# Kernel optimization log

Hardware: AMD Instinct MI355X
Metric: run time of the kernel (lower is better)

## Reference

```python
import jax, jax.numpy as jnp
import numpy as np

B, S, N, D, C, H = 256, 256, 128, 256, 512, 4  # batch, seq, mem_slots, mem_dim, controller_dim, heads
HD = D // H


def setup_inputs() -> dict:
    key = jax.random.key(0)
    ks = jax.random.split(key, 12)
    sc = 0.02
    p = lambda k, shape: (jax.random.normal(k, shape, jnp.float32) * sc)
    return {
        "input_seq": jax.random.normal(ks[0], (B, S, D), jnp.float32),
        "memory_init": jax.random.normal(ks[1], (N, D), jnp.float32) * (np.sqrt(6.0 / (N + D)) / np.sqrt(3.0)),
        # LSTM (torch gate order i, f, g, o)
        "W_ih": p(ks[2], (4 * C, D)), "W_hh": p(ks[3], (4 * C, C)),
        "b_ih": jnp.zeros((4 * C,), jnp.float32), "b_hh": jnp.zeros((4 * C,), jnp.float32),
        # heads
        "W_read": p(ks[4], (D, C)), "b_read": jnp.zeros((D,), jnp.float32),
        "W_write": p(ks[5], (2 * D, C)), "b_write": jnp.zeros((2 * D,), jnp.float32),
        "W_erase": p(ks[6], (D, C)), "b_erase": jnp.zeros((D,), jnp.float32),
        # MultiheadAttention packed in-proj (q,k,v) + out-proj
        "W_in": p(ks[7], (3 * D, D)), "b_in": jnp.zeros((3 * D,), jnp.float32),
        "W_out": p(ks[8], (D, D)), "b_out": jnp.zeros((D,), jnp.float32),
        # gates
        "W_rg": p(ks[9], (1, C)), "b_rg": jnp.zeros((1,), jnp.float32),
        "W_wg": p(ks[10], (1, C)), "b_wg": jnp.zeros((1,), jnp.float32),
    }


def reference(input_seq, memory_init, W_ih, W_hh, b_ih, b_hh,
              W_read, b_read, W_write, b_write, W_erase, b_erase,
              W_in, b_in, W_out, b_out, W_rg, b_rg, W_wg, b_wg):
    b, s, d = input_seq.shape
    Wq, Wk, Wv = jnp.split(W_in, 3, axis=0)
    bq, bk, bv = jnp.split(b_in, 3)
    inv_sqrt_hd = 1.0 / np.sqrt(HD)

    mem0 = jnp.broadcast_to(memory_init, (b,) + memory_init.shape)
    h0 = jnp.zeros((b, C), input_seq.dtype)
    c0 = jnp.zeros((b, C), input_seq.dtype)

    def step(carry, x_t):
        h, c, mem = carry  # h,c: [B,C]; mem: [B,N,D]
        # LSTM cell (torch gate order i,f,g,o)
        gates = x_t @ W_ih.T + b_ih + h @ W_hh.T + b_hh
        i, f, g, o = jnp.split(gates, 4, axis=-1)
        c = jax.nn.sigmoid(f) * c + jax.nn.sigmoid(i) * jnp.tanh(g)
        h = jax.nn.sigmoid(o) * jnp.tanh(c)
        # --- read: MHA(query=read_key, key=value=memory) ---
        rk = h @ W_read.T + b_read                      # [B,D]
        q = (rk @ Wq.T + bq).reshape(b, H, HD)          # [B,H,hd]
        k = (mem @ Wk.T + bk).reshape(b, -1, H, HD)     # [B,N,H,hd]
        v = (mem @ Wv.T + bv).reshape(b, -1, H, HD)
        scores = jnp.einsum('bhd,bnhd->bhn', q, k) * inv_sqrt_hd
        attn = jax.nn.softmax(scores, axis=-1)          # [B,H,N]
        ctx = jnp.einsum('bhn,bnhd->bhd', attn, v).reshape(b, d)
        read_out = ctx @ W_out.T + b_out
        read_gate = jax.nn.sigmoid(h @ W_rg.T + b_rg)   # [B,1]
        read = read_gate * read_out
        # --- write: erase/add ---
        wp = h @ W_write.T + b_write
        write_key, write_val = wp[:, :d], wp[:, d:]
        erase_vec = jax.nn.sigmoid(h @ W_erase.T + b_erase)  # [B,D]
        write_gate = jax.nn.sigmoid(h @ W_wg.T + b_wg)       # [B,1]
        wa = jax.nn.softmax(jnp.einsum('bd,bnd->bn', write_key, mem), axis=-1)  # [B,N]
        ew = wa[:, :, None]                                   # [B,N,1]
        mem = mem * (1.0 - ew * erase_vec[:, None, :]) + write_gate[:, None, :] * (ew * write_val[:, None, :])
        return (h, c, mem), x_t + read

    (hT, cT, memT), outs = jax.lax.scan(step, (h0, c0, mem0), jnp.swapaxes(input_seq, 0, 1))
    output_sequence = jnp.swapaxes(outs, 0, 1)  # [B,S,D]
    return output_sequence, memT
```

## Files before the change

### kernel.cpp

```cpp
#include <hip/hip_runtime.h>

#define S_LEN 256
#define B_SZ  256
#define N_MEM 128
#define D_DIM 256
#define C_DIM 512
#define NBLK  256
#define PROJS 1792
#define AGENT __HIP_MEMORY_SCOPE_AGENT

typedef __bf16 bf16x8 __attribute__((ext_vector_type(8)));
typedef unsigned short ushort4v __attribute__((ext_vector_type(4)));
typedef float floatx4 __attribute__((ext_vector_type(4)));
typedef float floatx2 __attribute__((ext_vector_type(2)));

__device__ __forceinline__ unsigned short f2bf(float f){
  unsigned u = __float_as_uint(f);
  u += 0x7FFFu + ((u >> 16) & 1u);
  return (unsigned short)(u >> 16);
}
__device__ __forceinline__ float bf2f(unsigned short v){
  return __uint_as_float(((unsigned)v) << 16);
}
__device__ __forceinline__ float sigm(float x){ return 1.f/(1.f + __expf(-x)); }
__device__ __forceinline__ floatx4 mfma16(bf16x8 a, bf16x8 b, floatx4 c){
  return __builtin_amdgcn_mfma_f32_16x16x32_bf16(a, b, c, 0, 0, 0);
}

__device__ __forceinline__ int msw(int n, int d){
  return (n << 8) + ((((d >> 2) ^ (n & 7)) << 2) | (d & 3));
}

__device__ __forceinline__ unsigned ald32(const void* p){
  return __hip_atomic_load((const unsigned*)p, __ATOMIC_RELAXED, AGENT);
}
__device__ __forceinline__ unsigned long long ald64(const void* p){
  return __hip_atomic_load((const unsigned long long*)p, __ATOMIC_RELAXED, AGENT);
}
__device__ __forceinline__ void ast32(void* p, unsigned v){
  __hip_atomic_store((unsigned*)p, v, __ATOMIC_RELAXED, AGENT);
}
__device__ __forceinline__ void ast64(void* p, unsigned long long v){
  __hip_atomic_store((unsigned long long*)p, v, __ATOMIC_RELAXED, AGENT);
}
__device__ __forceinline__ void sst16(void* p, unsigned short v){
  asm volatile("global_store_short %0, %1, off sc1" :: "v"(p), "v"(v) : "memory");
}

struct V16 { floatx4 v0,v1,v2,v3,v4,v5,v6,v7,v8,v9,v10,v11,v12,v13,v14,v15; };
#define BC(xx) __builtin_bit_cast(bf16x8, xx)

__device__ __forceinline__ V16 cload16(const unsigned short* base){
  V16 r;
  asm volatile(
    "global_load_dwordx4 %0, %16, off sc1\n\t"
    "global_load_dwordx4 %1, %16, off offset:64 sc1\n\t"
    "global_load_dwordx4 %2, %16, off offset:128 sc1\n\t"
    "global_load_dwordx4 %3, %16, off offset:192 sc1\n\t"
    "global_load_dwordx4 %4, %16, off offset:256 sc1\n\t"
    "global_load_dwordx4 %5, %16, off offset:320 sc1\n\t"
    "global_load_dwordx4 %6, %16, off offset:384 sc1\n\t"
    "global_load_dwordx4 %7, %16, off offset:448 sc1\n\t"
    "global_load_dwordx4 %8, %16, off offset:512 sc1\n\t"
    "global_load_dwordx4 %9, %16, off offset:576 sc1\n\t"
    "global_load_dwordx4 %10, %16, off offset:640 sc1\n\t"
    "global_load_dwordx4 %11, %16, off offset:704 sc1\n\t"
    "global_load_dwordx4 %12, %16, off offset:768 sc1\n\t"
    "global_load_dwordx4 %13, %16, off offset:832 sc1\n\t"
    "global_load_dwordx4 %14, %16, off offset:896 sc1\n\t"
    "global_load_dwordx4 %15, %16, off offset:960 sc1\n\t"
    "s_waitcnt vmcnt(0)"
    : "=&v"(r.v0), "=&v"(r.v1), "=&v"(r.v2), "=&v"(r.v3),
      "=&v"(r.v4), "=&v"(r.v5), "=&v"(r.v6), "=&v"(r.v7),
      "=&v"(r.v8), "=&v"(r.v9), "=&v"(r.v10), "=&v"(r.v11),
      "=&v"(r.v12), "=&v"(r.v13), "=&v"(r.v14), "=&v"(r.v15)
    : "v"(base)
    : "memory");
  __builtin_amdgcn_sched_barrier(0);
  return r;
}

__device__ __forceinline__ void cload16_issue(const unsigned short* base, floatx4 r[16]){
  asm volatile(
    "global_load_dwordx4 %0, %16, off sc1\n\t"
    "global_load_dwordx4 %1, %16, off offset:64 sc1\n\t"
    "global_load_dwordx4 %2, %16, off offset:128 sc1\n\t"
    "global_load_dwordx4 %3, %16, off offset:192 sc1\n\t"
    "global_load_dwordx4 %4, %16, off offset:256 sc1\n\t"
    "global_load_dwordx4 %5, %16, off offset:320 sc1\n\t"
    "global_load_dwordx4 %6, %16, off offset:384 sc1\n\t"
    "global_load_dwordx4 %7, %16, off offset:448 sc1\n\t"
    "global_load_dwordx4 %8, %16, off offset:512 sc1\n\t"
    "global_load_dwordx4 %9, %16, off offset:576 sc1\n\t"
    "global_load_dwordx4 %10, %16, off offset:640 sc1\n\t"
    "global_load_dwordx4 %11, %16, off offset:704 sc1\n\t"
    "global_load_dwordx4 %12, %16, off offset:768 sc1\n\t"
    "global_load_dwordx4 %13, %16, off offset:832 sc1\n\t"
    "global_load_dwordx4 %14, %16, off offset:896 sc1\n\t"
    "global_load_dwordx4 %15, %16, off offset:960 sc1"
    : "=&v"(r[0]), "=&v"(r[1]), "=&v"(r[2]), "=&v"(r[3]),
      "=&v"(r[4]), "=&v"(r[5]), "=&v"(r[6]), "=&v"(r[7]),
      "=&v"(r[8]), "=&v"(r[9]), "=&v"(r[10]), "=&v"(r[11]),
      "=&v"(r[12]), "=&v"(r[13]), "=&v"(r[14]), "=&v"(r[15])
    : "v"(base)
    : "memory");
}
__device__ __forceinline__ void cwait16(floatx4 r[16]){
  asm volatile("s_waitcnt vmcnt(0)"
    : "+v"(r[0]), "+v"(r[1]), "+v"(r[2]), "+v"(r[3]),
      "+v"(r[4]), "+v"(r[5]), "+v"(r[6]), "+v"(r[7]),
      "+v"(r[8]), "+v"(r[9]), "+v"(r[10]), "+v"(r[11]),
      "+v"(r[12]), "+v"(r[13]), "+v"(r[14]), "+v"(r[15])
    :: "memory");
  __builtin_amdgcn_sched_barrier(0);
}


__global__ __launch_bounds__(256) void p0_xbf(const float* __restrict__ x,
                                              unsigned short* __restrict__ xbf){
  int idx = (blockIdx.x*256 + threadIdx.x)*4;
  floatx4 f = *(const floatx4*)(x + idx);
  ushort4v u;
  u[0]=f2bf(f[0]); u[1]=f2bf(f[1]); u[2]=f2bf(f[2]); u[3]=f2bf(f[3]);
  *(ushort4v*)(xbf + idx) = u;
}

__global__ __launch_bounds__(256) void p1_wg(const float* __restrict__ Wih,
                                             const float* __restrict__ Whh,
                                             unsigned short* __restrict__ Wg){
  int idx = blockIdx.x*256 + threadIdx.x;
  int n = idx / 768, k = idx - n*768;
  float v = (k < 256) ? Wih[n*256 + k] : Whh[n*512 + (k-256)];
  Wg[idx] = f2bf(v);
}

__global__ __launch_bounds__(256) void p2_T(const float* __restrict__ Win,
                                            const float* __restrict__ Wread,
                                            const float* __restrict__ bread,
                                            const float* __restrict__ bin,
                                            float* __restrict__ T, float* __restrict__ rq){
  if (blockIdx.x < 512){
    int idx = blockIdx.x*256 + threadIdx.x;
    int e = idx >> 9, cc = idx & 511;
    float acc = 0.f;
    for (int dp = 0; dp < 256; ++dp) acc += Win[e*256 + dp] * Wread[dp*512 + cc];
    T[idx] = acc;
  } else {
    int e = threadIdx.x;
    float acc = bin[e];
    for (int dp = 0; dp < 256; ++dp) acc += bread[dp] * Win[e*256 + dp];
    rq[e] = acc;
  }
}

__global__ __launch_bounds__(256) void p3_w2(const float* __restrict__ Win,
                                             const float* __restrict__ Wwrite,
                                             const float* __restrict__ Werase,
                                             const float* __restrict__ Wrg,
                                             const float* __restrict__ Wwg,
                                             const float* __restrict__ bwrite,
                                             const float* __restrict__ berase,
                                             const float* __restrict__ brg,
                                             const float* __restrict__ bwg,
                                             const float* __restrict__ T,
                                             const float* __restrict__ rq,
                                             unsigned short* __restrict__ W2,
                                             float* __restrict__ bias2){
  int bid = blockIdx.x;
  if (bid < 2048){
    int idx = bid*256 + threadIdx.x;
    int j = idx >> 9, cc = idx & 511;
    int h = j >> 8, d = j & 255;
    float acc = 0.f;
    const float* wk = Win + (256 + h*64)*256 + d;
    const float* tp = T + (h*64)*512 + cc;
    for (int i = 0; i < 64; ++i) acc += wk[i*256] * tp[i*512];
    W2[(size_t)j*512 + cc] = f2bf(acc);
  } else if (bid < 2048 + 1568){
    int idx = (bid - 2048)*256 + threadIdx.x;
    int r = idx >> 9, cc = idx & 511;
    float v;
    if      (r < 512) v = Wwrite[r*512 + cc];
    else if (r < 768) v = Werase[(r-512)*512 + cc];
    else if (r == 768) v = Wrg[cc];
    else if (r == 769) v = Wwg[cc];
    else v = 0.f;
    W2[(size_t)(1024 + r)*512 + cc] = f2bf(v);
  } else {
    int j = (bid - 2048 - 1568)*256 + threadIdx.x;
    if (j >= 1808) return;
    float v;
    if (j < 1024){
      int h = j >> 8, d = j & 255;
      float acc = 0.f;
      for (int i = 0; i < 64; ++i) acc += rq[h*64+i] * Win[(256 + h*64 + i)*256 + d];
      v = acc;
    }
    else if (j < 1536) v = bwrite[j - 1024];
    else if (j < 1792) v = berase[j - 1536];
    else if (j == 1792) v = brg[0];
    else if (j == 1793) v = bwg[0];
    else v = 0.f;
    bias2[j] = v;
  }
}

__global__ __launch_bounds__(256) void p4_fold(const float* __restrict__ Win,
                                               const float* __restrict__ Wout,
                                               const float* __restrict__ bout,
                                               const float* __restrict__ bin,
                                               unsigned short* __restrict__ Fold,
                                               float* __restrict__ bout2){
  if (blockIdx.x < 1024){
    int idx = blockIdx.x*256 + threadIdx.x;
    int dp = idx >> 10, j = idx & 1023;
    int h = j & 3, d = j >> 2;
    float acc = 0.f;
    const float* wv = Win + (512 + h*64)*256 + d;
    const float* wo = Wout + dp*256 + h*64;
    for (int i = 0; i < 64; ++i) acc += wv[i*256] * wo[i];
    Fold[(size_t)dp*1024 + j] = f2bf(acc);
  } else {
    int dp = threadIdx.x;
    float acc = bout[dp];
    for (int e = 0; e < 256; ++e) acc += Wout[dp*256 + e] * bin[512 + e];
    bout2[dp] = acc;
  }
}

__global__ __launch_bounds__(256) void p5_init(const float* __restrict__ bih,
                                               const float* __restrict__ bhh,
                                               float* __restrict__ biasg,
                                               float* __restrict__ c,
                                               unsigned short* __restrict__ h0){
  int idx = blockIdx.x*256 + threadIdx.x;
  c[idx] = 0.f; h0[idx] = 0;
  if (idx < 2048) biasg[idx] = bih[idx] + bhh[idx];
}

__device__ __forceinline__ void gbarg(unsigned* cnt, unsigned target){
  __syncthreads();
  if (threadIdx.x == 0){
    __hip_atomic_fetch_add(cnt, 1u, __ATOMIC_RELAXED, AGENT);
    while (__hip_atomic_load(cnt, __ATOMIC_RELAXED, AGENT) < target)
      __builtin_amdgcn_s_sleep(1);
  }
  __builtin_amdgcn_sched_barrier(0);
  __syncthreads();
}


__device__ __forceinline__ void do_readout(int mt, int dt, int t,
                                           const unsigned short* __restrict__ mctx,
                                           const unsigned short* __restrict__ Fold,
                                           const float* __restrict__ rgb,
                                           const float* __restrict__ bout2,
                                           const float* __restrict__ x,
                                           float* __restrict__ out, int lane){
  const int lm = lane & 15, lk = (lane >> 4) * 8;
  const unsigned short* ap = mctx + (size_t)(mt*16 + lm)*1024 + lk;
  const unsigned short* bp = Fold + (size_t)(dt*16 + lm)*1024 + lk;
  const int r0 = mt*16 + ((lane >> 4) << 2);
  const float rg0 = __uint_as_float(ald32(&rgb[r0]));
  const float rg1 = __uint_as_float(ald32(&rgb[r0+1]));
  const float rg2 = __uint_as_float(ald32(&rgb[r0+2]));
  const float rg3 = __uint_as_float(ald32(&rgb[r0+3]));
  V16 a0 = cload16(ap);
  V16 a1 = cload16(ap + 512);
  const bf16x8 av[16] = {BC(a0.v0),BC(a0.v1),BC(a0.v2),BC(a0.v3),BC(a0.v4),BC(a0.v5),BC(a0.v6),BC(a0.v7),
                         BC(a0.v8),BC(a0.v9),BC(a0.v10),BC(a0.v11),BC(a0.v12),BC(a0.v13),BC(a0.v14),BC(a0.v15)};
  const bf16x8 bv[16] = {BC(a1.v0),BC(a1.v1),BC(a1.v2),BC(a1.v3),BC(a1.v4),BC(a1.v5),BC(a1.v6),BC(a1.v7),
                         BC(a1.v8),BC(a1.v9),BC(a1.v10),BC(a1.v11),BC(a1.v12),BC(a1.v13),BC(a1.v14),BC(a1.v15)};
  floatx4 acc = {0,0,0,0};
  #pragma unroll
  for (int kt = 0; kt < 16; ++kt)
    acc = mfma16(av[kt], *(const bf16x8*)(bp + kt*32), acc);
  #pragma unroll
  for (int kt = 0; kt < 16; ++kt)
    acc = mfma16(bv[kt], *(const bf16x8*)(bp + 512 + kt*32), acc);
  const int dp = dt*16 + lm;
  const float bo = bout2[dp];
  const float rg[4] = {rg0, rg1, rg2, rg3};
  #pragma unroll
  for (int q = 0; q < 4; ++q){
    const int bb = r0 + q;
    const size_t oi = ((size_t)bb * S_LEN + (t-1)) * D_DIM + dp;
    out[oi] = x[oi] + rg[q] * (acc[q] + bo);
  }
}

__global__ __launch_bounds__(512, 2) void kmain(
    const float* __restrict__ x,
    const unsigned short* __restrict__ xbf,
    const unsigned short* __restrict__ Wg,
    const float* __restrict__ biasg,
    const unsigned short* __restrict__ W2, const float* __restrict__ bias2,
    const unsigned short* __restrict__ Fold, const float* __restrict__ bout2,
    float* __restrict__ cbuf,
    unsigned short* __restrict__ h0buf, unsigned short* __restrict__ h1buf,
    unsigned short* __restrict__ projB, unsigned short* __restrict__ mctx,
    float* __restrict__ rgbuf, const float* __restrict__ mem0,
    float* __restrict__ memT, float* __restrict__ out,
    unsigned* __restrict__ barcnt)
{
  const int bid = blockIdx.x, tid = threadIdx.x;
  const int lane = tid & 63, wave = tid >> 6;
  const int lm = lane & 15, lk = (lane >> 4) * 8;

  __shared__ float memF[32768];
  __shared__ float scU[5][512];
  __shared__ float qkW[5][256];
  __shared__ float er[256];
  __shared__ float wvs[256];
  __shared__ float attT[128][8];
  __shared__ float hL[512];
  __shared__ float wgS;
  float (*ga)[16][32] = (float (*)[16][32])&scU[0][0];

  const int r = bid >> 4, uc = bid & 15, u0 = uc*32;
  unsigned* gcnt = barcnt + r*64;

  for (int i = tid; i < 32768; i += 512){
    const int n = i >> 8, d = i & 255;
    memF[msw(n, d)] = mem0[i];
  }

  unsigned nbar = 0;
  const unsigned short* hr = h0buf;
  unsigned short* hw = h1buf;
  const int g = wave >> 1, colh = wave & 1;
  const int row = r*16 + lm;
  const int slot = uc*8 + wave;

  floatx4 hq[16];
  bf16x8 xfr[8];
  cload16_issue(hr + (size_t)row*C_DIM + lk, hq);
  {
    const unsigned short* ax = xbf + ((size_t)row*S_LEN + 0)*D_DIM + lk;
    #pragma unroll
    for (int kt = 0; kt < 8; ++kt) xfr[kt] = *(const bf16x8*)(ax + kt*32);
  }

  for (int t = 0; t < S_LEN; ++t){
    {
      const unsigned short* wb = Wg + (size_t)(g*512 + u0 + colh*16 + lm)*768 + lk;
      cwait16(hq);
      floatx4 acc = {0,0,0,0};
      #pragma unroll
      for (int kt = 0; kt < 8; ++kt)
        acc = mfma16(xfr[kt], *(const bf16x8*)(wb + kt*32), acc);
      #pragma unroll
      for (int kt = 0; kt < 16; ++kt)
        acc = mfma16(BC(hq[kt]), *(const bf16x8*)(wb + 256 + kt*32), acc);
      const int rr0 = (lane >> 4) << 2;
      #pragma unroll
      for (int q = 0; q < 4; ++q) ga[g][rr0+q][colh*16 + lm] = acc[q];
      __syncthreads();
      if (tid < 256){
        const int ri = tid >> 4, cp = (tid & 15) * 2;
        const int b = r*16 + ri, u = u0 + cp;
        floatx2 bg0 = *(const floatx2*)&biasg[u];
        floatx2 bg1 = *(const floatx2*)&biasg[512 + u];
        floatx2 bg2 = *(const floatx2*)&biasg[1024 + u];
        floatx2 bg3 = *(const floatx2*)&biasg[1536 + u];
        const float gi0 = ga[0][ri][cp]   + bg0[0];
        const float gf0 = ga[1][ri][cp]   + bg1[0];
        const float gg0 = ga[2][ri][cp]   + bg2[0];
        const float go0 = ga[3][ri][cp]   + bg3[0];
        const float gi1 = ga[0][ri][cp+1] + bg0[1];
        const float gf1 = ga[1][ri][cp+1] + bg1[1];
        const float gg1 = ga[2][ri][cp+1] + bg2[1];
        const float go1 = ga[3][ri][cp+1] + bg3[1];
        const int ci2 = b*512 + u;
        floatx2 cv = *(const floatx2*)&cbuf[ci2];
        const float cn0 = sigm(gf0) * cv[0] + sigm(gi0) * tanhf(gg0);
        const float cn1 = sigm(gf1) * cv[1] + sigm(gi1) * tanhf(gg1);
        floatx2 cw; cw[0] = cn0; cw[1] = cn1;
        *(floatx2*)&cbuf[ci2] = cw;
        const unsigned hv2 = (unsigned)f2bf(sigm(go0) * tanhf(cn0))
                           | ((unsigned)f2bf(sigm(go1) * tanhf(cn1)) << 16);
        ast32((unsigned*)hw + (ci2 >> 1), hv2);
      }
    }
    gbarg(gcnt, (++nbar)*16u);
    {
      if (slot < 112){
        const int nt = slot;
        const unsigned short* ap = hw + (size_t)(r*16 + lm)*512 + lk;
        const unsigned short* bp = W2 + (size_t)(nt*16 + lm)*512 + lk;
        V16 av16 = cload16(ap);
        const bf16x8 av[16] = {BC(av16.v0),BC(av16.v1),BC(av16.v2),BC(av16.v3),BC(av16.v4),BC(av16.v5),BC(av16.v6),BC(av16.v7),
                               BC(av16.v8),BC(av16.v9),BC(av16.v10),BC(av16.v11),BC(av16.v12),BC(av16.v13),BC(av16.v14),BC(av16.v15)};
        floatx4 acc = {0,0,0,0};
        #pragma unroll
        for (int kt = 0; kt < 16; ++kt)
          acc = mfma16(av[kt], *(const bf16x8*)(bp + kt*32), acc);
        const int r0 = r*16 + ((lane >> 4) << 2);
        const int cc = nt*16 + lm;
        const float bv = bias2[cc];
        const bool sg = (cc >= 1536);
        #pragma unroll
        for (int q = 0; q < 4; ++q){
          float v = acc[q] + bv;
          if (sg) v = sigm(v);
          sst16(&projB[(size_t)(r0 + q)*PROJS + cc], f2bf(v));
        }
      } else if (t >= 1){
        do_readout(r, slot - 112, t, mctx, Fold, rgbuf, bout2, x, out, lane);
      }
    }
    gbarg(gcnt, (++nbar)*16u);
    {
      const unsigned long long* p64 = (const unsigned long long*)(projB + (size_t)bid*PROJS);
      if (tid < 448){
        unsigned long long u2 = ald64(p64 + tid);
        float e0 = bf2f((unsigned short)(u2 & 0xFFFFu));
        float e1 = bf2f((unsigned short)((u2 >> 16) & 0xFFFFu));
        float e2 = bf2f((unsigned short)((u2 >> 32) & 0xFFFFu));
        float e3 = bf2f((unsigned short)(u2 >> 48));
        const int j = tid*4;
        if (j < 1024){ float* q = &qkW[j>>8][j&255]; q[0]=e0; q[1]=e1; q[2]=e2; q[3]=e3; }
        else if (j < 1280){ float* q = &qkW[4][j-1024]; q[0]=e0; q[1]=e1; q[2]=e2; q[3]=e3; }
        else if (j < 1536){ float* q = &wvs[j-1280]; q[0]=e0; q[1]=e1; q[2]=e2; q[3]=e3; }
        else { float* q = &er[j-1536]; q[0]=e0; q[1]=e1; q[2]=e2; q[3]=e3; }
      } else {
        const int i = tid - 448;
        const unsigned long long* h64 = (const unsigned long long*)(hw + (size_t)bid*C_DIM);
        unsigned long long a = ald64(h64 + 2*i), b = ald64(h64 + 2*i + 1);
        float* q = &hL[i*8];
        q[0]=bf2f((unsigned short)(a & 0xFFFFu)); q[1]=bf2f((unsigned short)((a>>16)&0xFFFFu));
        q[2]=bf2f((unsigned short)((a>>32)&0xFFFFu)); q[3]=bf2f((unsigned short)(a>>48));
        q[4]=bf2f((unsigned short)(b & 0xFFFFu)); q[5]=bf2f((unsigned short)((b>>16)&0xFFFFu));
        q[6]=bf2f((unsigned short)((b>>32)&0xFFFFu)); q[7]=bf2f((unsigned short)(b>>48));
      }
      __syncthreads();
      if (wave >= 6){
        const int rowW = 1792 + (wave - 6);
        const unsigned short* wrow = W2 + (size_t)rowW*512 + lane*8;
        const float* hp = &hL[lane*8];
        float s = 0.f;
        #pragma unroll
        for (int c = 0; c < 8; ++c) s += hp[c] * bf2f(wrow[c]);
        #pragma unroll
        for (int off = 32; off; off >>= 1) s += __shfl_xor(s, off);
        if (lane == 0){
          const float v = sigm(s + bias2[rowW]);
          if (wave == 6) ast32(&rgbuf[bid], __float_as_uint(v));
          else wgS = v;
        }
      }
      {
        const int n = tid & 127, quarter = tid >> 7, db = quarter*64;
        const int c7 = n & 7;
        const float* mrow = &memF[n << 8];
        floatx4 A0={0,0,0,0},A1={0,0,0,0},A2={0,0,0,0},A3={0,0,0,0},A4={0,0,0,0};
        #pragma unroll 4
        for (int i = 0; i < 64; i += 4){
          floatx4 m4 = *(const floatx4*)(mrow + ((((db+i)>>2) ^ c7) << 2));
          floatx4 q0 = *(const floatx4*)&qkW[0][db+i];
          floatx4 q1 = *(const floatx4*)&qkW[1][db+i];
          floatx4 q2 = *(const floatx4*)&qkW[2][db+i];
          floatx4 q3 = *(const floatx4*)&qkW[3][db+i];
          floatx4 qw = *(const floatx4*)&qkW[4][db+i];
          A0 += m4*q0; A1 += m4*q1; A2 += m4*q2; A3 += m4*q3; A4 += m4*qw;
        }
        scU[0][tid] = A0[0]+A0[1]+A0[2]+A0[3];
        scU[1][tid] = A1[0]+A1[1]+A1[2]+A1[3];
        scU[2][tid] = A2[0]+A2[1]+A2[2]+A2[3];
        scU[3][tid] = A3[0]+A3[1]+A3[2]+A3[3];
        scU[4][tid] = A4[0]+A4[1]+A4[2]+A4[3];
      }
      __syncthreads();
      if (tid < 128){
        #pragma unroll
        for (int j = 0; j < 5; ++j){
          float v = scU[j][tid] + scU[j][tid+128] + scU[j][tid+256] + scU[j][tid+384];
          scU[j][tid] = (j < 4) ? v * 0.125f : v;
        }
      }
      __syncthreads();
      {
        const int w = tid >> 6, l = tid & 63;
        if (w < 5){
          const int j = w;
          float v0 = scU[j][l], v1 = scU[j][l + 64];
          float mx = fmaxf(v0, v1);
          #pragma unroll
          for (int off = 32; off; off >>= 1) mx = fmaxf(mx, __shfl_xor(mx, off));
          float e0 = __expf(v0 - mx), e1 = __expf(v1 - mx);
          float sm = e0 + e1;
          #pragma unroll
          for (int off = 32; off; off >>= 1) sm += __shfl_xor(sm, off);
          float inv = 1.f / sm;
          attT[l][j] = e0 * inv; attT[l + 64][j] = e1 * inv;
        }
      }
      __syncthreads();
      {
        const int tn = (t+1 < S_LEN) ? t+1 : t;
        const unsigned short* ax = xbf + ((size_t)row*S_LEN + tn)*D_DIM + lk;
        #pragma unroll
        for (int kt = 0; kt < 8; ++kt) xfr[kt] = *(const bf16x8*)(ax + kt*32);
        cload16_issue(hw + (size_t)row*C_DIM + lk, hq);
      }
      {
        const float wgv = wgS;
        const int dlow = lane & 7, ng = lane >> 3;
        const int dblk = wave*8 + dlow;
        const int pblk = dblk ^ ng;
        const int d4 = dblk*4;
        floatx4 er4 = *(const floatx4*)&er[d4];
        floatx4 wv4 = *(const floatx4*)&wvs[d4];
        floatx4 A0={0,0,0,0},A1={0,0,0,0},A2={0,0,0,0},A3={0,0,0,0};
        #pragma unroll 4
        for (int k = 0; k < 16; ++k){
          const int n = ng + k*8;
          float* maddr = &memF[(n << 8) + (pblk << 2)];
          floatx4 m = *(const floatx4*)maddr;
          floatx4 a4 = *(const floatx4*)&attT[n][0];
          const float aw = attT[n][4];
          A0 += a4[0]*m; A1 += a4[1]*m; A2 += a4[2]*m; A3 += a4[3]*m;
          m = m * (1.f - aw*er4) + (wgv*aw) * wv4;
          *(floatx4*)maddr = m;
        }
        #pragma unroll
        for (int off = 8; off <= 32; off <<= 1){
          #pragma unroll
          for (int c = 0; c < 4; ++c){
            A0[c] += __shfl_xor(A0[c], off);
            A1[c] += __shfl_xor(A1[c], off);
            A2[c] += __shfl_xor(A2[c], off);
            A3[c] += __shfl_xor(A3[c], off);
          }
        }
        if (ng == 0){
          unsigned long long* mrow2 = (unsigned long long*)(mctx + (size_t)bid*1024);
          #pragma unroll
          for (int dd = 0; dd < 4; ++dd){
            const unsigned lo = (unsigned)f2bf(A0[dd]) | ((unsigned)f2bf(A1[dd]) << 16);
            const unsigned hi = (unsigned)f2bf(A2[dd]) | ((unsigned)f2bf(A3[dd]) << 16);
            ast64(mrow2 + d4 + dd, (unsigned long long)lo | ((unsigned long long)hi << 32));
          }
        }
      }
    }
    unsigned short* tmp = (unsigned short*)hr; hr = hw; hw = tmp;
  }
  gbarg(gcnt, (++nbar)*16u);
  if (wave == 0)
    do_readout(r, uc, S_LEN, mctx, Fold, rgbuf, bout2, x, out, lane);
  for (int i = tid; i < 32768; i += 512){
    const int n = i >> 8, d = i & 255;
    memT[(size_t)bid * 32768 + i] = memF[msw(n, d)];
  }
}


extern "C" void kernel_launch(void* const* d_in, const int* in_sizes, int n_in,
                              void* d_out, int out_size, void* d_ws, size_t ws_size,
                              hipStream_t stream){
  const float* x      = (const float*)d_in[0];
  const float* mem0   = (const float*)d_in[1];
  const float* Wih    = (const float*)d_in[2];
  const float* Whh    = (const float*)d_in[3];
  const float* bih    = (const float*)d_in[4];
  const float* bhh    = (const float*)d_in[5];
  const float* Wread  = (const float*)d_in[6];
  const float* bread  = (const float*)d_in[7];
  const float* Wwrite = (const float*)d_in[8];
  const float* bwrite = (const float*)d_in[9];
  const float* Werase = (const float*)d_in[10];
  const float* berase = (const float*)d_in[11];
  const float* Win    = (const float*)d_in[12];
  const float* bin    = (const float*)d_in[13];
  const float* Wout   = (const float*)d_in[14];
  const float* bout   = (const float*)d_in[15];
  const float* Wrg    = (const float*)d_in[16];
  const float* brg    = (const float*)d_in[17];
  const float* Wwg    = (const float*)d_in[18];
  const float* bwg    = (const float*)d_in[19];
  float* out = (float*)d_out;
  float* memT = out + (size_t)B_SZ * S_LEN * D_DIM;

  char* ws = (char*)d_ws;
  size_t off = 0;
  auto alloc = [&](size_t bytes) -> void* {
    void* p = ws + off; off += (bytes + 511) & ~(size_t)511; return p;
  };
  unsigned short* xbf  = (unsigned short*)alloc((size_t)B_SZ*S_LEN*D_DIM*2);
  unsigned short* Wg   = (unsigned short*)alloc((size_t)2048*768*2);
  unsigned short* W2   = (unsigned short*)alloc((size_t)1808*512*2);
  unsigned short* Fold = (unsigned short*)alloc((size_t)256*1024*2);
  float* T     = (float*)alloc((size_t)256*512*4);
  float* rq    = (float*)alloc(256*4);
  float* bias2 = (float*)alloc(1808*4);
  float* bout2 = (float*)alloc(256*4);
  float* biasg = (float*)alloc(2048*4);
  float* cbuf  = (float*)alloc((size_t)256*512*4);
  unsigned short* h0 = (unsigned short*)alloc((size_t)256*512*2);
  unsigned short* h1 = (unsigned short*)alloc((size_t)256*512*2);
  unsigned short* projB = (unsigned short*)alloc((size_t)256*PROJS*2);
  unsigned short* mctx = (unsigned short*)alloc((size_t)256*1024*2);
  float* rgbuf = (float*)alloc(256*4);
  unsigned* barcnt = (unsigned*)alloc(16384);
  (void)ws_size; (void)in_sizes; (void)n_in; (void)out_size;

  (void)hipMemsetAsync(barcnt, 0, 16384, stream);
  p0_xbf <<<16384, 256, 0, stream>>>(x, xbf);
  p1_wg  <<<6144, 256, 0, stream>>>(Wih, Whh, Wg);
  p2_T   <<<513,  256, 0, stream>>>(Win, Wread, bread, bin, T, rq);
  p3_w2  <<<3624, 256, 0, stream>>>(Win, Wwrite, Werase, Wrg, Wwg, bwrite, berase, brg, bwg, T, rq, W2, bias2);
  p4_fold<<<1025, 256, 0, stream>>>(Win, Wout, bout, bin, Fold, bout2);
  p5_init<<<512,  256, 0, stream>>>(bih, bhh, biasg, cbuf, h0);

  kmain<<<NBLK, 512, 0, stream>>>(x, xbf, Wg, biasg, W2, bias2, Fold, bout2,
                                  cbuf, h0, h1, projB, mctx, rgbuf, mem0, memT, out, barcnt);
}
```

Before: 8.487 ms.

## Stage hidden state in swizzled LDS once per step instead of per-wave global loads

After the first grid barrier, each block cooperatively loads its 16 rows of the new hidden state from global memory into a swizzled shared-memory tile. The LSTM gate GEMM, the projection GEMM and the gate dot products then read h from LDS, replacing the repeated per-wave coherent global loads and the async h prefetch. This also drops the double-buffered global h, folds shared buffers into one arena, and switches the score reduction to a 4-lanes-per-slot shuffle with padded q storage. In exchange, each step gains an extra cooperative load plus __syncthreads, and the h prefetch that used to overlap the memory update is gone.

```diff
diff --git a/kernel.cpp b/kernel.cpp
--- a/kernel.cpp
+++ b/kernel.cpp
@@ -7,10 +7,12 @@
 #define C_DIM 512
 #define NBLK  256
 #define PROJS 1792
+#define QKS   272
 #define AGENT __HIP_MEMORY_SCOPE_AGENT
 
 typedef __bf16 bf16x8 __attribute__((ext_vector_type(8)));
 typedef unsigned short ushort4v __attribute__((ext_vector_type(4)));
+typedef unsigned short ushort8v __attribute__((ext_vector_type(8)));
 typedef float floatx4 __attribute__((ext_vector_type(4)));
 typedef float floatx2 __attribute__((ext_vector_type(2)));
 
@@ -29,6 +31,9 @@
 
 __device__ __forceinline__ int msw(int n, int d){
   return (n << 8) + ((((d >> 2) ^ (n & 7)) << 2) | (d & 3));
+}
+__device__ __forceinline__ int hsw(int row, int blk){
+  return row*512 + ((blk ^ (row & 7)) << 3);
 }
 
 __device__ __forceinline__ unsigned ald32(const void* p){
@@ -78,41 +83,6 @@
     : "memory");
   __builtin_amdgcn_sched_barrier(0);
   return r;
-}
-
-__device__ __forceinline__ void cload16_issue(const unsigned short* base, floatx4 r[16]){
-  asm volatile(
-    "global_load_dwordx4 %0, %16, off sc1\n\t"
-    "global_load_dwordx4 %1, %16, off offset:64 sc1\n\t"
-    "global_load_dwordx4 %2, %16, off offset:128 sc1\n\t"
-    "global_load_dwordx4 %3, %16, off offset:192 sc1\n\t"
-    "global_load_dwordx4 %4, %16, off offset:256 sc1\n\t"
-    "global_load_dwordx4 %5, %16, off offset:320 sc1\n\t"
-    "global_load_dwordx4 %6, %16, off offset:384 sc1\n\t"
-    "global_load_dwordx4 %7, %16, off offset:448 sc1\n\t"
-    "global_load_dwordx4 %8, %16, off offset:512 sc1\n\t"
-    "global_load_dwordx4 %9, %16, off offset:576 sc1\n\t"
-    "global_load_dwordx4 %10, %16, off offset:640 sc1\n\t"
-    "global_load_dwordx4 %11, %16, off offset:704 sc1\n\t"
-    "global_load_dwordx4 %12, %16, off offset:768 sc1\n\t"
-    "global_load_dwordx4 %13, %16, off offset:832 sc1\n\t"
-    "global_load_dwordx4 %14, %16, off offset:896 sc1\n\t"
-    "global_load_dwordx4 %15, %16, off offset:960 sc1"
-    : "=&v"(r[0]), "=&v"(r[1]), "=&v"(r[2]), "=&v"(r[3]),
-      "=&v"(r[4]), "=&v"(r[5]), "=&v"(r[6]), "=&v"(r[7]),
-      "=&v"(r[8]), "=&v"(r[9]), "=&v"(r[10]), "=&v"(r[11]),
-      "=&v"(r[12]), "=&v"(r[13]), "=&v"(r[14]), "=&v"(r[15])
-    : "v"(base)
-    : "memory");
-}
-__device__ __forceinline__ void cwait16(floatx4 r[16]){
-  asm volatile("s_waitcnt vmcnt(0)"
-    : "+v"(r[0]), "+v"(r[1]), "+v"(r[2]), "+v"(r[3]),
-      "+v"(r[4]), "+v"(r[5]), "+v"(r[6]), "+v"(r[7]),
-      "+v"(r[8]), "+v"(r[9]), "+v"(r[10]), "+v"(r[11]),
-      "+v"(r[12]), "+v"(r[13]), "+v"(r[14]), "+v"(r[15])
-    :: "memory");
-  __builtin_amdgcn_sched_barrier(0);
 }
 
 
@@ -250,13 +220,14 @@
 }
 
 
-__device__ __forceinline__ void do_readout(int mt, int dt, int t,
-                                           const unsigned short* __restrict__ mctx,
-                                           const unsigned short* __restrict__ Fold,
-                                           const float* __restrict__ rgb,
-                                           const float* __restrict__ bout2,
-                                           const float* __restrict__ x,
-                                           float* __restrict__ out, int lane){
+__device__ __forceinline__ void do_readout_hst(const unsigned short* hSTp,
+                                               int mt, int dt, int t,
+                                               const unsigned short* __restrict__ mctx,
+                                               const unsigned short* __restrict__ Fold,
+                                               const float* __restrict__ rgb,
+                                               const float* __restrict__ bout2,
+                                               const float* __restrict__ x,
+                                               float* __restrict__ out, int lane){
   const int lm = lane & 15, lk = (lane >> 4) * 8;
   const unsigned short* ap = mctx + (size_t)(mt*16 + lm)*1024 + lk;
   const unsigned short* bp = Fold + (size_t)(dt*16 + lm)*1024 + lk;
@@ -297,7 +268,7 @@
     const unsigned short* __restrict__ W2, const float* __restrict__ bias2,
     const unsigned short* __restrict__ Fold, const float* __restrict__ bout2,
     float* __restrict__ cbuf,
-    unsigned short* __restrict__ h0buf, unsigned short* __restrict__ h1buf,
+    unsigned short* __restrict__ hgl,
     unsigned short* __restrict__ projB, unsigned short* __restrict__ mctx,
     float* __restrict__ rgbuf, const float* __restrict__ mem0,
     float* __restrict__ memT, float* __restrict__ out,
@@ -306,16 +277,18 @@
   const int bid = blockIdx.x, tid = threadIdx.x;
   const int lane = tid & 63, wave = tid >> 6;
   const int lm = lane & 15, lk = (lane >> 4) * 8;
+  const int lkg = lane >> 4;
 
   __shared__ float memF[32768];
-  __shared__ float scU[5][512];
-  __shared__ float qkW[5][256];
-  __shared__ float er[256];
-  __shared__ float wvs[256];
-  __shared__ float attT[128][8];
-  __shared__ float hL[512];
-  __shared__ float wgS;
-  float (*ga)[16][32] = (float (*)[16][32])&scU[0][0];
+  __shared__ unsigned short hST[8192];
+  __shared__ float arena[3552];
+  float (*ga)[16][32] = (float (*)[16][32])&arena[0];
+  float* qkA  = &arena[0];
+  float* erA  = &arena[1360];
+  float* wvA  = &arena[1616];
+  float* scP  = &arena[1872];
+  float* attT = &arena[2512];
+  float* wgSp = &arena[3536];
 
   const int r = bid >> 4, uc = bid & 15, u0 = uc*32;
   unsigned* gcnt = barcnt + r*64;
@@ -324,35 +297,38 @@
     const int n = i >> 8, d = i & 255;
     memF[msw(n, d)] = mem0[i];
   }
+  {
+    unsigned long long* hz = (unsigned long long*)hST;
+    #pragma unroll
+    for (int k = 0; k < 4; ++k) hz[tid*4 + k] = 0ull;
+  }
 
   unsigned nbar = 0;
-  const unsigned short* hr = h0buf;
-  unsigned short* hw = h1buf;
-  const int g = wave >> 1, colh = wave & 1;
   const int row = r*16 + lm;
   const int slot = uc*8 + wave;
 
-  floatx4 hq[16];
   bf16x8 xfr[8];
-  cload16_issue(hr + (size_t)row*C_DIM + lk, hq);
   {
     const unsigned short* ax = xbf + ((size_t)row*S_LEN + 0)*D_DIM + lk;
     #pragma unroll
     for (int kt = 0; kt < 8; ++kt) xfr[kt] = *(const bf16x8*)(ax + kt*32);
   }
+  __syncthreads();
 
   for (int t = 0; t < S_LEN; ++t){
     {
-      const unsigned short* wb = Wg + (size_t)(g*512 + u0 + colh*16 + lm)*768 + lk;
-      cwait16(hq);
+      const unsigned short* wb = Wg + (size_t)(wave/2*512 + u0 + (wave&1)*16 + lm)*768 + lk;
       floatx4 acc = {0,0,0,0};
       #pragma unroll
       for (int kt = 0; kt < 8; ++kt)
         acc = mfma16(xfr[kt], *(const bf16x8*)(wb + kt*32), acc);
       #pragma unroll
-      for (int kt = 0; kt < 16; ++kt)
-        acc = mfma16(BC(hq[kt]), *(const bf16x8*)(wb + 256 + kt*32), acc);
-      const int rr0 = (lane >> 4) << 2;
+      for (int kt = 0; kt < 16; ++kt){
+        bf16x8 ha = *(const bf16x8*)&hST[hsw(lm, kt*4 + lkg)];
+        acc = mfma16(ha, *(const bf16x8*)(wb + 256 + kt*32), acc);
+      }
+      const int g = wave >> 1, colh = wave & 1;
+      const int rr0 = lkg << 2;
       #pragma unroll
       for (int q = 0; q < 4; ++q) ga[g][rr0+q][colh*16 + lm] = acc[q];
       __syncthreads();
@@ -379,23 +355,33 @@
         *(floatx2*)&cbuf[ci2] = cw;
         const unsigned hv2 = (unsigned)f2bf(sigm(go0) * tanhf(cn0))
                            | ((unsigned)f2bf(sigm(go1) * tanhf(cn1)) << 16);
-        ast32((unsigned*)hw + (ci2 >> 1), hv2);
+        ast32((unsigned*)hgl + (ci2 >> 1), hv2);
       }
     }
     gbarg(gcnt, (++nbar)*16u);
     {
+      #pragma unroll
+      for (int b2 = 0; b2 < 2; ++b2){
+        const int blkid = tid*2 + b2;
+        const int hrow = blkid >> 6, blk = blkid & 63;
+        const unsigned short* gsrc = hgl + (size_t)(r*16 + hrow)*512 + blk*8;
+        unsigned long long lo = ald64(gsrc);
+        unsigned long long hi = ald64(gsrc + 4);
+        const int a = hsw(hrow, blk);
+        *(unsigned long long*)&hST[a]     = lo;
+        *(unsigned long long*)&hST[a + 4] = hi;
+      }
+      __syncthreads();
       if (slot < 112){
         const int nt = slot;
-        const unsigned short* ap = hw + (size_t)(r*16 + lm)*512 + lk;
         const unsigned short* bp = W2 + (size_t)(nt*16 + lm)*512 + lk;
-        V16 av16 = cload16(ap);
-        const bf16x8 av[16] = {BC(av16.v0),BC(av16.v1),BC(av16.v2),BC(av16.v3),BC(av16.v4),BC(av16.v5),BC(av16.v6),BC(av16.v7),
-                               BC(av16.v8),BC(av16.v9),BC(av16.v10),BC(av16.v11),BC(av16.v12),BC(av16.v13),BC(av16.v14),BC(av16.v15)};
         floatx4 acc = {0,0,0,0};
         #pragma unroll
-        for (int kt = 0; kt < 16; ++kt)
-          acc = mfma16(av[kt], *(const bf16x8*)(bp + kt*32), acc);
-        const int r0 = r*16 + ((lane >> 4) << 2);
+        for (int kt = 0; kt < 16; ++kt){
+          bf16x8 av = *(const bf16x8*)&hST[hsw(lm, kt*4 + lkg)];
+          acc = mfma16(av, *(const bf16x8*)(bp + kt*32), acc);
+        }
+        const int r0 = r*16 + (lkg << 2);
         const int cc = nt*16 + lm;
         const float bv = bias2[cc];
         const bool sg = (cc >= 1536);
@@ -406,7 +392,7 @@
           sst16(&projB[(size_t)(r0 + q)*PROJS + cc], f2bf(v));
         }
       } else if (t >= 1){
-        do_readout(r, slot - 112, t, mctx, Fold, rgbuf, bout2, x, out, lane);
+        do_readout_hst(hST, r, slot - 112, t, mctx, Fold, rgbuf, bout2, x, out, lane);
       }
     }
     gbarg(gcnt, (++nbar)*16u);
@@ -419,71 +405,71 @@
         float e2 = bf2f((unsigned short)((u2 >> 32) & 0xFFFFu));
         float e3 = bf2f((unsigned short)(u2 >> 48));
         const int j = tid*4;
-        if (j < 1024){ float* q = &qkW[j>>8][j&255]; q[0]=e0; q[1]=e1; q[2]=e2; q[3]=e3; }
-        else if (j < 1280){ float* q = &qkW[4][j-1024]; q[0]=e0; q[1]=e1; q[2]=e2; q[3]=e3; }
-        else if (j < 1536){ float* q = &wvs[j-1280]; q[0]=e0; q[1]=e1; q[2]=e2; q[3]=e3; }
-        else { float* q = &er[j-1536]; q[0]=e0; q[1]=e1; q[2]=e2; q[3]=e3; }
-      } else {
-        const int i = tid - 448;
-        const unsigned long long* h64 = (const unsigned long long*)(hw + (size_t)bid*C_DIM);
-        unsigned long long a = ald64(h64 + 2*i), b = ald64(h64 + 2*i + 1);
-        float* q = &hL[i*8];
-        q[0]=bf2f((unsigned short)(a & 0xFFFFu)); q[1]=bf2f((unsigned short)((a>>16)&0xFFFFu));
-        q[2]=bf2f((unsigned short)((a>>32)&0xFFFFu)); q[3]=bf2f((unsigned short)(a>>48));
-        q[4]=bf2f((unsigned short)(b & 0xFFFFu)); q[5]=bf2f((unsigned short)((b>>16)&0xFFFFu));
-        q[6]=bf2f((unsigned short)((b>>32)&0xFFFFu)); q[7]=bf2f((unsigned short)(b>>48));
+        if (j < 1280){
+          const int qj = j >> 8, d = j & 255;
+          float* qd = &qkA[qj*QKS + d + ((d >> 6) << 2)];
+          qd[0]=e0; qd[1]=e1; qd[2]=e2; qd[3]=e3;
+        }
+        else if (j < 1536){ float* qd = &wvA[j-1280]; qd[0]=e0; qd[1]=e1; qd[2]=e2; qd[3]=e3; }
+        else { float* qd = &erA[j-1536]; qd[0]=e0; qd[1]=e1; qd[2]=e2; qd[3]=e3; }
       }
       __syncthreads();
       if (wave >= 6){
         const int rowW = 1792 + (wave - 6);
         const unsigned short* wrow = W2 + (size_t)rowW*512 + lane*8;
-        const float* hp = &hL[lane*8];
+        ushort8v hv = *(const ushort8v*)&hST[hsw(uc, lane)];
         float s = 0.f;
         #pragma unroll
-        for (int c = 0; c < 8; ++c) s += hp[c] * bf2f(wrow[c]);
+        for (int c = 0; c < 8; ++c) s += bf2f(hv[c]) * bf2f(wrow[c]);
         #pragma unroll
         for (int off = 32; off; off >>= 1) s += __shfl_xor(s, off);
         if (lane == 0){
           const float v = sigm(s + bias2[rowW]);
           if (wave == 6) ast32(&rgbuf[bid], __float_as_uint(v));
-          else wgS = v;
+          else *wgSp = v;
         }
       }
       {
-        const int n = tid & 127, quarter = tid >> 7, db = quarter*64;
+        const int n = tid >> 2, q = tid & 3, db = q*64;
         const int c7 = n & 7;
         const float* mrow = &memF[n << 8];
         floatx4 A0={0,0,0,0},A1={0,0,0,0},A2={0,0,0,0},A3={0,0,0,0},A4={0,0,0,0};
         #pragma unroll 4
         for (int i = 0; i < 64; i += 4){
           floatx4 m4 = *(const floatx4*)(mrow + ((((db+i)>>2) ^ c7) << 2));
-          floatx4 q0 = *(const floatx4*)&qkW[0][db+i];
-          floatx4 q1 = *(const floatx4*)&qkW[1][db+i];
-          floatx4 q2 = *(const floatx4*)&qkW[2][db+i];
-          floatx4 q3 = *(const floatx4*)&qkW[3][db+i];
-          floatx4 qw = *(const floatx4*)&qkW[4][db+i];
+          const int qo = db + (q << 2) + i;
+          floatx4 q0 = *(const floatx4*)&qkA[0*QKS + qo];
+          floatx4 q1 = *(const floatx4*)&qkA[1*QKS + qo];
+          floatx4 q2 = *(const floatx4*)&qkA[2*QKS + qo];
+          floatx4 q3 = *(const floatx4*)&qkA[3*QKS + qo];
+          floatx4 qw = *(const floatx4*)&qkA[4*QKS + qo];
           A0 += m4*q0; A1 += m4*q1; A2 += m4*q2; A3 += m4*q3; A4 += m4*qw;
         }
-        scU[0][tid] = A0[0]+A0[1]+A0[2]+A0[3];
-        scU[1][tid] = A1[0]+A1[1]+A1[2]+A1[3];
-        scU[2][tid] = A2[0]+A2[1]+A2[2]+A2[3];
-        scU[3][tid] = A3[0]+A3[1]+A3[2]+A3[3];
-        scU[4][tid] = A4[0]+A4[1]+A4[2]+A4[3];
-      }
-      __syncthreads();
-      if (tid < 128){
+        float s0 = A0[0]+A0[1]+A0[2]+A0[3];
+        float s1 = A1[0]+A1[1]+A1[2]+A1[3];
+        float s2 = A2[0]+A2[1]+A2[2]+A2[3];
+        float s3 = A3[0]+A3[1]+A3[2]+A3[3];
+        float s4 = A4[0]+A4[1]+A4[2]+A4[3];
         #pragma unroll
-        for (int j = 0; j < 5; ++j){
-          float v = scU[j][tid] + scU[j][tid+128] + scU[j][tid+256] + scU[j][tid+384];
-          scU[j][tid] = (j < 4) ? v * 0.125f : v;
+        for (int off = 1; off <= 2; off <<= 1){
+          s0 += __shfl_xor(s0, off); s1 += __shfl_xor(s1, off);
+          s2 += __shfl_xor(s2, off); s3 += __shfl_xor(s3, off);
+          s4 += __shfl_xor(s4, off);
+        }
+        if (q == 0){
+          scP[0*128 + n] = s0 * 0.125f;
+          scP[1*128 + n] = s1 * 0.125f;
+          scP[2*128 + n] = s2 * 0.125f;
+          scP[3*128 + n] = s3 * 0.125f;
+          scP[4*128 + n] = s4;
         }
       }
       __syncthreads();
       {
-        const int w = tid >> 6, l = tid & 63;
+        const int w = wave, l = lane;
         if (w < 5){
           const int j = w;
-          float v0 = scU[j][l], v1 = scU[j][l + 64];
+          float v0 = scP[j*128 + l], v1 = scP[j*128 + l + 64];
           float mx = fmaxf(v0, v1);
           #pragma unroll
           for (int off = 32; off; off >>= 1) mx = fmaxf(mx, __shfl_xor(mx, off));
@@ -492,7 +478,7 @@
           #pragma unroll
           for (int off = 32; off; off >>= 1) sm += __shfl_xor(sm, off);
           float inv = 1.f / sm;
-          attT[l][j] = e0 * inv; attT[l + 64][j] = e1 * inv;
+          attT[l*8 + j] = e0 * inv; attT[(l + 64)*8 + j] = e1 * inv;
         }
       }
       __syncthreads();
@@ -501,24 +487,23 @@
         const unsigned short* ax = xbf + ((size_t)row*S_LEN + tn)*D_DIM + lk;
         #pragma unroll
         for (int kt = 0; kt < 8; ++kt) xfr[kt] = *(const bf16x8*)(ax + kt*32);
-        cload16_issue(hw + (size_t)row*C_DIM + lk, hq);
       }
       {
-        const float wgv = wgS;
+        const float wgv = *wgSp;
         const int dlow = lane & 7, ng = lane >> 3;
         const int dblk = wave*8 + dlow;
         const int pblk = dblk ^ ng;
         const int d4 = dblk*4;
-        floatx4 er4 = *(const floatx4*)&er[d4];
-        floatx4 wv4 = *(const floatx4*)&wvs[d4];
+        floatx4 er4 = *(const floatx4*)&erA[d4];
+        floatx4 wv4 = *(const floatx4*)&wvA[d4];
         floatx4 A0={0,0,0,0},A1={0,0,0,0},A2={0,0,0,0},A3={0,0,0,0};
         #pragma unroll 4
         for (int k = 0; k < 16; ++k){
           const int n = ng + k*8;
           float* maddr = &memF[(n << 8) + (pblk << 2)];
           floatx4 m = *(const floatx4*)maddr;
-          floatx4 a4 = *(const floatx4*)&attT[n][0];
-          const float aw = attT[n][4];
+          floatx4 a4 = *(const floatx4*)&attT[n*8];
+          const float aw = attT[n*8 + 4];
           A0 += a4[0]*m; A1 += a4[1]*m; A2 += a4[2]*m; A3 += a4[3]*m;
           m = m * (1.f - aw*er4) + (wgv*aw) * wv4;
           *(floatx4*)maddr = m;
@@ -544,11 +529,10 @@
         }
       }
     }
-    unsigned short* tmp = (unsigned short*)hr; hr = hw; hw = tmp;
   }
   gbarg(gcnt, (++nbar)*16u);
   if (wave == 0)
-    do_readout(r, uc, S_LEN, mctx, Fold, rgbuf, bout2, x, out, lane);
+    do_readout_hst(hST, r, uc, S_LEN, mctx, Fold, rgbuf, bout2, x, out, lane);
   for (int i = tid; i < 32768; i += 512){
     const int n = i >> 8, d = i & 255;
     memT[(size_t)bid * 32768 + i] = memF[msw(n, d)];
@@ -598,7 +582,6 @@
   float* biasg = (float*)alloc(2048*4);
   float* cbuf  = (float*)alloc((size_t)256*512*4);
   unsigned short* h0 = (unsigned short*)alloc((size_t)256*512*2);
-  unsigned short* h1 = (unsigned short*)alloc((size_t)256*512*2);
   unsigned short* projB = (unsigned short*)alloc((size_t)256*PROJS*2);
   unsigned short* mctx = (unsigned short*)alloc((size_t)256*1024*2);
   float* rgbuf = (float*)alloc(256*4);
@@ -614,5 +597,5 @@
   p5_init<<<512,  256, 0, stream>>>(bih, bhh, biasg, cbuf, h0);
 
   kmain<<<NBLK, 512, 0, stream>>>(x, xbf, Wg, biasg, W2, bias2, Fold, bout2,
-                                  cbuf, h0, h1, projB, mctx, rgbuf, mem0, memT, out, barcnt);
-}
+                                  cbuf, h0, projB, mctx, rgbuf, mem0, memT, out, barcnt);
+}
```

Result: slower. 9.823 ms (+15.7%).
